# Kernel tuning notes

Hardware: AMD Instinct MI355X
Metric: run time of the kernel (lower is better)

Reference implementation:

```python
import jax, jax.numpy as jnp
import numpy as np

B, S, E, H = 2, 2048, 2048, 16
D = E // H  # head_dim = 128


def setup_inputs() -> dict:
    key = jax.random.key(0)
    ks = jax.random.split(key, 7)
    x = jax.random.normal(ks[0], (B, S, E), dtype=jnp.float32)
    cos = jax.random.uniform(ks[1], (S, D), dtype=jnp.float32)
    sin = jax.random.uniform(ks[2], (S, D), dtype=jnp.float32)
    scale = 1.0 / np.sqrt(E)
    Wq = jax.random.normal(ks[3], (E, E), dtype=jnp.float32) * scale
    Wk = jax.random.normal(ks[4], (E, E), dtype=jnp.float32) * scale
    Wv = jax.random.normal(ks[5], (E, E), dtype=jnp.float32) * scale
    Wo = jax.random.normal(ks[6], (E, E), dtype=jnp.float32) * scale
    return {"x": x, "cos": cos, "sin": sin, "Wq": Wq, "Wk": Wk, "Wv": Wv, "Wo": Wo}


def _apply_rope(t, cos, sin):
    # t: [B, S, H, D]; cos/sin: [S, D]. NeoX rotate-half.
    half = t.shape[-1] // 2
    rotate = jnp.concatenate([-t[..., half:], t[..., :half]], axis=-1)
    return t * cos[None, :, None, :] + rotate * sin[None, :, None, :]


def reference(x, cos, sin, Wq, Wk, Wv, Wo):
    b, s, e = x.shape
    q = (x @ Wq.T).reshape(b, s, H, D)
    k = (x @ Wk.T).reshape(b, s, H, D)
    v = (x @ Wv.T).reshape(b, s, H, D)
    q = _apply_rope(q, cos, sin).transpose(0, 2, 1, 3)  # [B,H,S,D]
    k = _apply_rope(k, cos, sin).transpose(0, 2, 1, 3)
    v = v.transpose(0, 2, 1, 3)
    scale = 1.0 / jnp.sqrt(jnp.asarray(D, dtype=x.dtype))
    scores = jnp.einsum("bhqd,bhkd->bhqk", q, k) * scale
    causal = jnp.tril(jnp.ones((s, s), dtype=bool))
    scores = jnp.where(causal[None, None], scores, jnp.asarray(-1e30, dtype=scores.dtype))
    attn = jax.nn.softmax(scores, axis=-1)
    out = jnp.einsum("bhqk,bhkd->bhqd", attn, v)  # [B,H,S,D]
    out = out.transpose(0, 2, 1, 3).reshape(b, s, e)
    return out @ Wo.T
```

## Files before the change

### kernel.cpp

```cpp
#include <hip/hip_runtime.h>
#include <stdint.h>

typedef unsigned short u16;
typedef __attribute__((ext_vector_type(8))) short short8;
typedef __attribute__((ext_vector_type(4))) float f32x4;
typedef __attribute__((ext_vector_type(16))) float f32x16;

#define B_ 2
#define S_ 2048
#define E_ 2048
#define H_ 16
#define D_ 128
#define M_ 4096

__device__ __forceinline__ u16 f2bf(float f) {
  unsigned u = __float_as_uint(f);
  u = u + 0x7FFFu + ((u >> 16) & 1u);
  return (u16)(u >> 16);
}
__device__ __forceinline__ float bf2f(u16 h) {
  return __uint_as_float(((unsigned)h) << 16);
}

#define GLD16(gp, lp) __builtin_amdgcn_global_load_lds(                      \
    (__attribute__((address_space(1))) void*)(gp),                           \
    (__attribute__((address_space(3))) void*)(lp), 16, 0, 0)

__global__ void cast_bf16(const float4* __restrict__ src, ushort4* __restrict__ dst, int n4) {
  int i = blockIdx.x * 256 + threadIdx.x;
  if (i < n4) {
    float4 v = src[i];
    ushort4 o;
    o.x = f2bf(v.x); o.y = f2bf(v.y); o.z = f2bf(v.z); o.w = f2bf(v.w);
    dst[i] = o;
  }
}

__global__ void cast4_bf16(const float4* __restrict__ w0, const float4* __restrict__ w1,
                           const float4* __restrict__ w2, const float4* __restrict__ w3,
                           ushort4* __restrict__ o0, ushort4* __restrict__ o1,
                           ushort4* __restrict__ o2, ushort4* __restrict__ o3, int n4) {
  const int i = blockIdx.x * 256 + threadIdx.x;
  if (i >= n4) return;
  const float4* s; ushort4* d;
  switch (blockIdx.y) {
    case 0: s = w0; d = o0; break;
    case 1: s = w1; d = o1; break;
    case 2: s = w2; d = o2; break;
    default: s = w3; d = o3; break;
  }
  float4 v = s[i];
  ushort4 o;
  o.x = f2bf(v.x); o.y = f2bf(v.y); o.z = f2bf(v.z); o.w = f2bf(v.w);
  d[i] = o;
}

template <int MODE>
__launch_bounds__(256, 2)
__global__ void gemm_bt(const u16* __restrict__ A, const u16* __restrict__ Bw,
                        void* __restrict__ Cp, int M, int N, int K) {
  __shared__ alignas(16) u16 As[128 * 32];
  __shared__ alignas(16) u16 Bs[128 * 32];
  const int tid = threadIdx.x;
  const int wave = tid >> 6, lane = tid & 63;
  const int m0 = blockIdx.y * 128, n0 = blockIdx.x * 128;
  const int wr = (wave >> 1) * 64, wc = (wave & 1) * 64;
  const int lrow = lane & 15, lk = (lane >> 4) * 8;
  f32x4 acc[4][4] = {};

  for (int k0 = 0; k0 < K; k0 += 32) {
#pragma unroll
    for (int q = 0; q < 2; ++q) {
      const int g = q * 4 + wave;
      const int c = g * 64 + lane;
      const int row = c >> 2, ch = (c & 3) * 8;
      GLD16(A + (size_t)(m0 + row) * K + k0 + ch, &As[g * 512]);
      GLD16(Bw + (size_t)(n0 + row) * K + k0 + ch, &Bs[g * 512]);
    }
    __syncthreads();
    short8 a[4], b[4];
#pragma unroll
    for (int m = 0; m < 4; ++m) a[m] = *(const short8*)&As[(wr + m * 16 + lrow) * 32 + lk];
#pragma unroll
    for (int n = 0; n < 4; ++n) b[n] = *(const short8*)&Bs[(wc + n * 16 + lrow) * 32 + lk];
#pragma unroll
    for (int m = 0; m < 4; ++m)
#pragma unroll
      for (int n = 0; n < 4; ++n)
        acc[m][n] = __builtin_amdgcn_mfma_f32_16x16x32_bf16(a[m], b[n], acc[m][n], 0, 0, 0);
    __syncthreads();
  }

  const int rbase = (lane >> 4) * 4;
#pragma unroll
  for (int m = 0; m < 4; ++m)
#pragma unroll
    for (int n = 0; n < 4; ++n)
#pragma unroll
      for (int r = 0; r < 4; ++r) {
        const int mm = m0 + wr + m * 16 + rbase + r;
        const int nn = n0 + wc + n * 16 + lrow;
        const float v = acc[m][n][r];
        if (MODE == 0) {
          const size_t NXc = (size_t)B_ * S_ * E_;
          const int bb = mm >> 11, s = mm & (S_ - 1);
          const int tz = nn >> 11, nc = nn & 2047;
          const int h = nc >> 7, d = nc & (D_ - 1);
          ((u16*)Cp)[(size_t)tz * NXc + (((size_t)bb * H_ + h) * S_ + s) * D_ + d] = f2bf(v);
        } else {
          ((float*)Cp)[(size_t)mm * N + nn] = v;
        }
      }
}

__global__ void rope2_k(u16* __restrict__ Qb, u16* __restrict__ Kb,
                        const float* __restrict__ cosT, const float* __restrict__ sinT) {
  const int y = blockIdx.y;
  u16* T = y ? Kb : Qb;
  const float sc = y ? 1.f : 0.12751744154f;
  const int idx = blockIdx.x * 256 + threadIdx.x;
  const int row = idx >> 3;
  const int d0 = (idx & 7) * 8;
  const int s = row & (S_ - 1);
  const size_t base = (size_t)row * D_;
  short8 lo = *(const short8*)&T[base + d0];
  short8 hv = *(const short8*)&T[base + d0 + 64];
  float c1v[8], s1v[8], c2v[8], s2v[8];
  *(float4*)&c1v[0] = *(const float4*)&cosT[s * D_ + d0];
  *(float4*)&c1v[4] = *(const float4*)&cosT[s * D_ + d0 + 4];
  *(float4*)&s1v[0] = *(const float4*)&sinT[s * D_ + d0];
  *(float4*)&s1v[4] = *(const float4*)&sinT[s * D_ + d0 + 4];
  *(float4*)&c2v[0] = *(const float4*)&cosT[s * D_ + d0 + 64];
  *(float4*)&c2v[4] = *(const float4*)&cosT[s * D_ + d0 + 68];
  *(float4*)&s2v[0] = *(const float4*)&sinT[s * D_ + d0 + 64];
  *(float4*)&s2v[4] = *(const float4*)&sinT[s * D_ + d0 + 68];
  short8 olo, ohi;
#pragma unroll
  for (int j = 0; j < 8; ++j) {
    const float x1 = bf2f((u16)lo[j]), x2 = bf2f((u16)hv[j]);
    olo[j] = (short)f2bf((x1 * c1v[j] - x2 * s1v[j]) * sc);
    ohi[j] = (short)f2bf((x2 * c2v[j] + x1 * s2v[j]) * sc);
  }
  *(short8*)&T[base + d0] = olo;
  *(short8*)&T[base + d0 + 64] = ohi;
}

__global__ void transpose64(const u16* __restrict__ V, u16* __restrict__ VT) {
  __shared__ alignas(16) u16 t[64][72];
  const int bh = blockIdx.z, st = blockIdx.y * 64, dt = blockIdx.x * 64;
  const u16* Vp = V + (size_t)bh * S_ * D_;
  u16* Tp = VT + (size_t)bh * D_ * S_;
  const int tid = threadIdx.x;
#pragma unroll
  for (int p = 0; p < 2; ++p) {
    const int idx = p * 256 + tid;
    const int r = idx >> 3, c8 = (idx & 7) * 8;
    *(short8*)&t[r][c8] = *(const short8*)&Vp[(size_t)(st + r) * D_ + dt + c8];
  }
  __syncthreads();
#pragma unroll
  for (int p = 0; p < 2; ++p) {
    const int idx = p * 256 + tid;
    const int dr = idx >> 3, s8 = (idx & 7) * 8;
    short8 v;
#pragma unroll
    for (int j = 0; j < 8; ++j) v[j] = t[s8 + j][dr];
    *(short8*)&Tp[(size_t)(dt + dr) * S_ + st + s8] = v;
  }
}

__launch_bounds__(512, 2)
__global__ void attn_fwd(const u16* __restrict__ Q, const u16* __restrict__ Kt,
                         const u16* __restrict__ VT, u16* __restrict__ Out) {
  __shared__ alignas(16) u16 SB[2][2][16384];
  __shared__ float MLB[4][64][2];
  const int tid = threadIdx.x, wave = tid >> 6, lane = tid & 63;
  const int grp = wave >> 2, w4 = wave & 3;
  const int hw = blockIdx.x;
  const int lid = (hw & 7) * 32 + (hw >> 3);
  const int p = lid & 7, bh = lid >> 3;
  const int bb = bh >> 4, h = bh & 15;
  const u16* Qh = Q + (size_t)bh * S_ * D_;
  const u16* Kh = Kt + (size_t)bh * S_ * D_;
  const u16* Vh = VT + (size_t)bh * D_ * S_;
  const int l31 = lane & 31, hi = lane >> 5;

  auto stage = [&](int buf, int kv0) {
#pragma unroll
    for (int pp = 0; pp < 4; ++pp) {
      const int g = pp * 4 + w4;
      const int c = g * 64 + lane;
      const int srow = c >> 4, dch = c & 15;
      GLD16(Kh + (size_t)(kv0 + srow) * D_ + ((dch ^ (srow & 7)) * 8), &SB[grp][buf][g * 512]);
      const int drow = c >> 3, sch = c & 7;
      GLD16(Vh + (size_t)drow * S_ + kv0 + ((sch ^ (drow & 7)) * 8), &SB[grp][buf][8192 + g * 512]);
    }
  };

  float* obuf = (float*)&SB[1][0][0];

  const int qts[2] = {15 - p, p};
#pragma unroll 1
  for (int seg = 0; seg < 2; ++seg) {
    const int t = qts[seg];
    const int iters = t + 1;
    const int q0 = t * 128 + w4 * 32;
    const int qg = q0 + l31;

    short8 qf[8];
#pragma unroll
    for (int m = 0; m < 8; ++m)
      qf[m] = *(const short8*)&Qh[(size_t)qg * D_ + m * 16 + hi * 8];

    f32x16 od[4] = {};
    float mr = 0.f, lsum = 0.f;

    stage(0, grp * 64);
    int cur = 0;

    for (int i = 0; i < iters; ++i) {
      __syncthreads();
      if (i + 1 < iters) stage(cur ^ 1, (2 * (i + 1) + grp) * 64);
      const int kv0 = (2 * i + grp) * 64;
      const u16* Kc = &SB[grp][cur][0];
      const u16* Vc = &SB[grp][cur][8192];

      f32x16 s0 = {}, s1 = {};
      __builtin_amdgcn_s_setprio(1);
#pragma unroll
      for (int m = 0; m < 8; ++m) {
        const int col = m * 16 + hi * 8;
        const int sw = (l31 & 7) << 3;
        short8 k0 = *(const short8*)&Kc[l31 * 128 + (col ^ sw)];
        short8 k1 = *(const short8*)&Kc[(32 + l31) * 128 + (col ^ sw)];
        s0 = __builtin_amdgcn_mfma_f32_32x32x16_bf16(k0, qf[m], s0, 0, 0, 0);
        s1 = __builtin_amdgcn_mfma_f32_32x32x16_bf16(k1, qf[m], s1, 0, 0, 0);
      }
      __builtin_amdgcn_s_setprio(0);

      if (kv0 + 63 > q0) {
#pragma unroll
        for (int r = 0; r < 16; ++r) {
          const int k0g = kv0 + (r & 3) + 8 * (r >> 2) + 4 * hi;
          if (k0g > qg)      s0[r] = -1e30f;
          if (k0g + 32 > qg) s1[r] = -1e30f;
        }
      }

      float mloc = s0[0];
#pragma unroll
      for (int r = 1; r < 16; ++r) mloc = fmaxf(mloc, s0[r]);
#pragma unroll
      for (int r = 0; r < 16; ++r) mloc = fmaxf(mloc, s1[r]);
      const float mx = fmaxf(mloc, __shfl_xor(mloc, 32));
      const bool need = !__all(mx <= mr + 8.f);
      float corr = 1.f;
      if (need) {
        const float mnew = fmaxf(mr, mx);
        corr = exp2f(mr - mnew);
        mr = mnew;
      }
      float sloc = 0.f;
#pragma unroll
      for (int r = 0; r < 16; ++r) { s0[r] = exp2f(s0[r] - mr); sloc += s0[r]; }
#pragma unroll
      for (int r = 0; r < 16; ++r) { s1[r] = exp2f(s1[r] - mr); sloc += s1[r]; }
      const float rsum = sloc + __shfl_xor(sloc, 32);
      lsum = lsum * corr + rsum;
      if (need) {
#pragma unroll
        for (int dt = 0; dt < 4; ++dt)
#pragma unroll
          for (int r = 0; r < 16; ++r) od[dt][r] *= corr;
      }

      unsigned W0[4][2], W1[4][2];
#pragma unroll
      for (int c = 0; c < 4; ++c)
#pragma unroll
        for (int pr = 0; pr < 2; ++pr) {
          asm("v_cvt_pk_bf16_f32 %0, %1, %2"
              : "=v"(W0[c][pr]) : "v"(s0[4 * c + 2 * pr]), "v"(s0[4 * c + 2 * pr + 1]));
          asm("v_cvt_pk_bf16_f32 %0, %1, %2"
              : "=v"(W1[c][pr]) : "v"(s1[4 * c + 2 * pr]), "v"(s1[4 * c + 2 * pr + 1]));
        }

      __builtin_amdgcn_s_setprio(1);
#pragma unroll
      for (int kk = 0; kk < 4; ++kk) {
        const int cown = 2 * (kk & 1) + hi, csend = 2 * (kk & 1) + 1 - hi;
        unsigned o0, o1, sd0, sd1;
        if (kk < 2) { o0 = W0[cown][0]; o1 = W0[cown][1]; sd0 = W0[csend][0]; sd1 = W0[csend][1]; }
        else        { o0 = W1[cown][0]; o1 = W1[cown][1]; sd0 = W1[csend][0]; sd1 = W1[csend][1]; }
        const unsigned r0 = (unsigned)__shfl_xor((int)sd0, 32);
        const unsigned r1 = (unsigned)__shfl_xor((int)sd1, 32);
        uint4 bw;
        if (hi == 0) bw = make_uint4(o0, o1, r0, r1);
        else         bw = make_uint4(r0, r1, o0, o1);
        const short8 pf = *(const short8*)&bw;
        const int slot = 2 * kk + hi;
#pragma unroll
        for (int dt = 0; dt < 4; ++dt) {
          const int row = dt * 32 + l31;
          const short8 vf = *(const short8*)&Vc[row * 64 + ((slot ^ (row & 7)) * 8)];
          od[dt] = __builtin_amdgcn_mfma_f32_32x32x16_bf16(vf, pf, od[dt], 0, 0, 0);
        }
      }
      __builtin_amdgcn_s_setprio(0);
      cur ^= 1;
    }

    __syncthreads();
    if (grp == 1) {
      MLB[w4][lane][0] = mr;
      MLB[w4][lane][1] = lsum;
#pragma unroll
      for (int dt = 0; dt < 4; ++dt)
#pragma unroll
        for (int r = 0; r < 16; ++r)
          obuf[(dt * 16 + r) * 256 + w4 * 64 + lane] = od[dt][r];
    }
    __syncthreads();
    if (grp == 0) {
      const float mB = MLB[w4][lane][0];
      const float lB = MLB[w4][lane][1];
      const float m = fmaxf(mr, mB);
      const float aA = exp2f(mr - m), aB = exp2f(mB - m);
      lsum = lsum * aA + lB * aB;
#pragma unroll
      for (int dt = 0; dt < 4; ++dt)
#pragma unroll
        for (int r = 0; r < 16; ++r)
          od[dt][r] = od[dt][r] * aA + obuf[(dt * 16 + r) * 256 + w4 * 64 + lane] * aB;

      const float inv = 1.f / lsum;
      const size_t obase = ((size_t)bb * S_ + qg) * E_ + h * D_;
#pragma unroll
      for (int dt = 0; dt < 4; ++dt)
#pragma unroll
        for (int g = 0; g < 4; ++g) {
          ushort4 w;
          w.x = f2bf(od[dt][4 * g + 0] * inv);
          w.y = f2bf(od[dt][4 * g + 1] * inv);
          w.z = f2bf(od[dt][4 * g + 2] * inv);
          w.w = f2bf(od[dt][4 * g + 3] * inv);
          *(ushort4*)&Out[obase + dt * 32 + 8 * g + 4 * hi] = w;
        }
    }
    __syncthreads();
  }
}

extern "C" void kernel_launch(void* const* d_in, const int* in_sizes, int n_in,
                              void* d_out, int out_size, void* d_ws, size_t ws_size,
                              hipStream_t stream) {
  const float* x    = (const float*)d_in[0];
  const float* cosT = (const float*)d_in[1];
  const float* sinT = (const float*)d_in[2];
  const float* Wq   = (const float*)d_in[3];
  const float* Wk   = (const float*)d_in[4];
  const float* Wv   = (const float*)d_in[5];
  const float* Wo   = (const float*)d_in[6];
  float* out = (float*)d_out;

  const size_t NX = (size_t)B_ * S_ * E_;
  const size_t NW = (size_t)E_ * E_;
  u16* ws  = (u16*)d_ws;
  u16* xb  = ws;
  u16* Wqb = xb + NX;
  u16* Wkb = Wqb + NW;
  u16* Wvb = Wkb + NW;
  u16* Wob = Wvb + NW;
  u16* Qb  = Wob + NW;
  u16* Kb  = Qb + NX;
  u16* Vb  = Kb + NX;
  u16* VTb = Vb + NX;
  u16* Ab  = VTb + NX;

  cast_bf16<<<(int)(NX / 4 / 256), 256, 0, stream>>>((const float4*)x, (ushort4*)xb, (int)(NX / 4));
  cast4_bf16<<<dim3((int)(NW / 4 / 256), 4), 256, 0, stream>>>(
      (const float4*)Wq, (const float4*)Wk, (const float4*)Wv, (const float4*)Wo,
      (ushort4*)Wqb, (ushort4*)Wkb, (ushort4*)Wvb, (ushort4*)Wob, (int)(NW / 4));

  gemm_bt<0><<<dim3(48, 32), 256, 0, stream>>>(xb, Wqb, Qb, M_, 3 * E_, E_);

  rope2_k<<<dim3((B_ * H_ * S_ * 8) / 256, 2), 256, 0, stream>>>(Qb, Kb, cosT, sinT);

  transpose64<<<dim3(D_ / 64, S_ / 64, B_ * H_), 256, 0, stream>>>(Vb, VTb);

  attn_fwd<<<dim3(256), 512, 0, stream>>>(Qb, Kb, VTb, Ab);

  gemm_bt<1><<<dim3(16, 32), 256, 0, stream>>>(Ab, Wob, out, M_, E_, E_);
}
```

Before: 289.7 us.

## Replace GEMM with 128x256 tile, triple-buffered K pipeline and XCD-aware block mapping

```diff
diff --git a/kernel.cpp b/kernel.cpp
--- a/kernel.cpp
+++ b/kernel.cpp
@@ -56,50 +56,97 @@
 }
 
 template <int MODE>
-__launch_bounds__(256, 2)
-__global__ void gemm_bt(const u16* __restrict__ A, const u16* __restrict__ Bw,
-                        void* __restrict__ Cp, int M, int N, int K) {
-  __shared__ alignas(16) u16 As[128 * 32];
-  __shared__ alignas(16) u16 Bs[128 * 32];
-  const int tid = threadIdx.x;
-  const int wave = tid >> 6, lane = tid & 63;
-  const int m0 = blockIdx.y * 128, n0 = blockIdx.x * 128;
-  const int wr = (wave >> 1) * 64, wc = (wave & 1) * 64;
-  const int lrow = lane & 15, lk = (lane >> 4) * 8;
+__launch_bounds__(512, 1)
+__global__ void gemm256(const u16* __restrict__ A, const u16* __restrict__ Bw,
+                        void* __restrict__ Cp, int M, int N, int K, int gx) {
+  __shared__ alignas(16) u16 LA[3][128 * 64];
+  __shared__ alignas(16) u16 LB[3][256 * 64];
+  const int tid = threadIdx.x, wave = tid >> 6, lane = tid & 63;
+  const int cpx = gridDim.x >> 3;
+  const int orig = blockIdx.x;
+  const int wg = (orig & 7) * cpx + (orig >> 3);
+  const int bx = wg % gx, by = wg / gx;
+  const int m0 = by * 128, n0 = bx * 256;
+  const int wm = (wave >> 2) * 64, wn = (wave & 3) * 64;
+  const int lrow = lane & 15, lq = lane >> 4;
+
+  auto stageA = [&](int buf, int kt) {
+    const int k0 = kt * 64;
+#pragma unroll
+    for (int i = 0; i < 2; ++i) {
+      const int c = i * 512 + tid;
+      const int row = c >> 3, k = c & 7;
+      GLD16(A + (size_t)(m0 + row) * K + k0 + ((k ^ (row & 7)) * 8),
+            &LA[buf][i * 4096 + wave * 512]);
+    }
+    {
+      const int c = tid;
+      const int row = c >> 3, k = c & 7;
+      GLD16(Bw + (size_t)(n0 + row) * K + k0 + ((k ^ (row & 7)) * 8),
+            &LB[buf][wave * 512]);
+    }
+  };
+  auto stageB = [&](int buf, int kt) {
+    const int k0 = kt * 64;
+#pragma unroll
+    for (int i = 1; i < 4; ++i) {
+      const int c = i * 512 + tid;
+      const int row = c >> 3, k = c & 7;
+      GLD16(Bw + (size_t)(n0 + row) * K + k0 + ((k ^ (row & 7)) * 8),
+            &LB[buf][i * 4096 + wave * 512]);
+    }
+  };
+
   f32x4 acc[4][4] = {};
-
-  for (int k0 = 0; k0 < K; k0 += 32) {
-#pragma unroll
-    for (int q = 0; q < 2; ++q) {
-      const int g = q * 4 + wave;
-      const int c = g * 64 + lane;
-      const int row = c >> 2, ch = (c & 3) * 8;
-      GLD16(A + (size_t)(m0 + row) * K + k0 + ch, &As[g * 512]);
-      GLD16(Bw + (size_t)(n0 + row) * K + k0 + ch, &Bs[g * 512]);
-    }
-    __syncthreads();
-    short8 a[4], b[4];
-#pragma unroll
-    for (int m = 0; m < 4; ++m) a[m] = *(const short8*)&As[(wr + m * 16 + lrow) * 32 + lk];
-#pragma unroll
-    for (int n = 0; n < 4; ++n) b[n] = *(const short8*)&Bs[(wc + n * 16 + lrow) * 32 + lk];
-#pragma unroll
-    for (int m = 0; m < 4; ++m)
-#pragma unroll
-      for (int n = 0; n < 4; ++n)
-        acc[m][n] = __builtin_amdgcn_mfma_f32_16x16x32_bf16(a[m], b[n], acc[m][n], 0, 0, 0);
-    __syncthreads();
-  }
-
-  const int rbase = (lane >> 4) * 4;
+  const int NT = K >> 6;
+  stageA(0, 0); stageB(0, 0);
+  stageA(1, 1); stageB(1, 1);
+
+  for (int t = 0; t < NT; ++t) {
+    if (t < NT - 1) { asm volatile("s_waitcnt vmcnt(6)" ::: "memory"); }
+    else           { asm volatile("s_waitcnt vmcnt(0)" ::: "memory"); }
+    __builtin_amdgcn_sched_barrier(0);
+    __builtin_amdgcn_s_barrier();
+    __builtin_amdgcn_sched_barrier(0);
+    const int cur = t % 3;
+    const int sb = (t + 2) % 3;
+    const bool dostage = (t + 2) < NT;
+
+#pragma unroll
+    for (int kk = 0; kk < 2; ++kk) {
+      if (dostage) { if (kk == 0) stageA(sb, t + 2); else stageB(sb, t + 2); }
+      short8 a[4], b[4];
+#pragma unroll
+      for (int m = 0; m < 4; ++m) {
+        const int row = wm + m * 16 + lrow;
+        const int c = kk * 4 + lq;
+        a[m] = *(const short8*)&LA[cur][row * 64 + ((c ^ (row & 7)) * 8)];
+      }
+#pragma unroll
+      for (int n = 0; n < 4; ++n) {
+        const int row = wn + n * 16 + lrow;
+        const int c = kk * 4 + lq;
+        b[n] = *(const short8*)&LB[cur][row * 64 + ((c ^ (row & 7)) * 8)];
+      }
+      __builtin_amdgcn_s_setprio(1);
+#pragma unroll
+      for (int m = 0; m < 4; ++m)
+#pragma unroll
+        for (int n = 0; n < 4; ++n)
+          acc[m][n] = __builtin_amdgcn_mfma_f32_16x16x32_bf16(a[m], b[n], acc[m][n], 0, 0, 0);
+      __builtin_amdgcn_s_setprio(0);
+    }
+  }
+
+  const int rbase = lq * 4;
 #pragma unroll
   for (int m = 0; m < 4; ++m)
 #pragma unroll
     for (int n = 0; n < 4; ++n)
 #pragma unroll
       for (int r = 0; r < 4; ++r) {
-        const int mm = m0 + wr + m * 16 + rbase + r;
-        const int nn = n0 + wc + n * 16 + lrow;
+        const int mm = m0 + wm + m * 16 + rbase + r;
+        const int nn = n0 + wn + n * 16 + lrow;
         const float v = acc[m][n][r];
         if (MODE == 0) {
           const size_t NXc = (size_t)B_ * S_ * E_;
@@ -175,7 +222,6 @@
   __shared__ alignas(16) u16 SB[2][2][16384];
   __shared__ float MLB[4][64][2];
   const int tid = threadIdx.x, wave = tid >> 6, lane = tid & 63;
-  const int grp = wave >> 2, w4 = wave & 3;
   const int hw = blockIdx.x;
   const int lid = (hw & 7) * 32 + (hw >> 3);
   const int p = lid & 7, bh = lid >> 3;
@@ -183,6 +229,7 @@
   const u16* Qh = Q + (size_t)bh * S_ * D_;
   const u16* Kh = Kt + (size_t)bh * S_ * D_;
   const u16* Vh = VT + (size_t)bh * D_ * S_;
+  const int grp = wave >> 2, w4 = wave & 3;
   const int l31 = lane & 31, hi = lane >> 5;
 
   auto stage = [&](int buf, int kv0) {
@@ -382,7 +429,7 @@
       (const float4*)Wq, (const float4*)Wk, (const float4*)Wv, (const float4*)Wo,
       (ushort4*)Wqb, (ushort4*)Wkb, (ushort4*)Wvb, (ushort4*)Wob, (int)(NW / 4));
 
-  gemm_bt<0><<<dim3(48, 32), 256, 0, stream>>>(xb, Wqb, Qb, M_, 3 * E_, E_);
+  gemm256<0><<<dim3(768), 512, 0, stream>>>(xb, Wqb, Qb, M_, 3 * E_, E_, 24);
 
   rope2_k<<<dim3((B_ * H_ * S_ * 8) / 256, 2), 256, 0, stream>>>(Qb, Kb, cosT, sinT);
 
@@ -390,5 +437,5 @@
 
   attn_fwd<<<dim3(256), 512, 0, stream>>>(Qb, Kb, VTb, Ab);
 
-  gemm_bt<1><<<dim3(16, 32), 256, 0, stream>>>(Ab, Wob, out, M_, E_, E_);
-}
+  gemm256<1><<<dim3(256), 512, 0, stream>>>(Ab, Wob, out, M_, E_, E_, 8);
+}
```

Measured after the change: 315.8 us. 1.09x slower.
